# Optimization experiments

Measured on AMD Instinct MI355X. Metric: run time of the kernel, lower is better.

Reference implementation:

```python
import jax, jax.numpy as jnp
import numpy as np

N = 100000      # nodes
E = 1600000     # edges
F_IN = 64       # node_features
F_OUT = 32      # output_size


def _cheb2(H, row, col, w_norm, theta, bias):
    # ChebConv K=2, sym normalization, lambda_max=2 (GCLSTM default):
    # L_hat = L - I = -D^{-1/2} A D^{-1/2}, so T0 = H, T1 = -A_norm H
    agg = jax.ops.segment_sum(w_norm[:, None] * H[col], row, num_segments=N)  # [N, F_OUT]
    return H @ theta[0] - agg @ theta[1] + bias


def setup_inputs() -> dict:
    key = jax.random.key(0)
    ks = jax.random.split(key, 24)
    inp = {}
    inp["x"] = jax.random.normal(ks[0], (N, F_IN), jnp.float32)
    inp["edge_index"] = jax.random.randint(ks[1], (2, E), 0, N)
    inp["edge_weight"] = jax.random.uniform(ks[2], (E,), jnp.float32)
    inp["h"] = jax.random.normal(ks[3], (N, F_OUT), jnp.float32)
    inp["c"] = jax.random.normal(ks[4], (N, F_OUT), jnp.float32)
    s_in = float(1.0 / np.sqrt(F_IN))
    s_out = float(1.0 / np.sqrt(F_OUT))
    i = 5
    for g in "ifco":
        inp[f"W_{g}"] = jax.random.uniform(ks[i], (F_IN, F_OUT), jnp.float32, -s_in, s_in); i += 1
        inp[f"b_{g}"] = jax.random.uniform(ks[i], (1, F_OUT), jnp.float32, -s_in, s_in); i += 1
        inp[f"theta_{g}"] = jax.random.uniform(ks[i], (2, F_OUT, F_OUT), jnp.float32, -s_out, s_out); i += 1
        inp[f"cb_{g}"] = jax.random.uniform(ks[i], (F_OUT,), jnp.float32, -s_out, s_out); i += 1
    inp["W_lin"] = jax.random.uniform(ks[i], (F_OUT, 1), jnp.float32, -s_out, s_out); i += 1
    inp["b_lin"] = jax.random.uniform(ks[i], (1,), jnp.float32, -s_out, s_out)
    return inp


def reference(x, edge_index, edge_weight, h, c,
              W_i, b_i, theta_i, cb_i,
              W_f, b_f, theta_f, cb_f,
              W_c, b_c, theta_c, cb_c,
              W_o, b_o, theta_o, cb_o,
              W_lin, b_lin):
    row, col = edge_index[0], edge_index[1]
    # symmetric normalization of edge weights (get_laplacian 'sym')
    deg = jax.ops.segment_sum(edge_weight, row, num_segments=N)
    dis = jnp.where(deg > 0, jax.lax.rsqrt(jnp.where(deg > 0, deg, 1.0)), 0.0)
    w_norm = dis[row] * edge_weight * dis[col]  # [E]
    # GCLSTM gates: input x through dense W, hidden h through ChebConv
    I = jax.nn.sigmoid(x @ W_i + _cheb2(h, row, col, w_norm, theta_i, cb_i) + b_i)
    Fg = jax.nn.sigmoid(x @ W_f + _cheb2(h, row, col, w_norm, theta_f, cb_f) + b_f)
    T = jnp.tanh(x @ W_c + _cheb2(h, row, col, w_norm, theta_c, cb_c) + b_c)
    C = Fg * c + I * T
    O = jax.nn.sigmoid(x @ W_o + _cheb2(h, row, col, w_norm, theta_o, cb_o) + b_o)
    H = O * jnp.tanh(C)
    # wrapper head: relu then Linear(out, 1)
    return jax.nn.relu(H) @ W_lin + b_lin  # [N, 1]
```

## Files before the change

### kernel.cpp

```cpp
#include <hip/hip_runtime.h>
#include <math.h>

#define NN 100000
#define NE 1600000
#define BSH 7
#define BMSK 127
#define NBUK 782
#define EPB 2048
#define NEB 782
#define CAPH 1536

typedef __attribute__((ext_vector_type(8))) short bf16x8;
typedef __attribute__((ext_vector_type(4))) float f32x4;

#define MFMA(A, B, C) __builtin_amdgcn_mfma_f32_16x16x32_bf16(A, B, C, 0, 0, 0)

__device__ __forceinline__ float sigm(float z) { return 1.0f / (1.0f + expf(-z)); }

__device__ __forceinline__ void split1(float v, unsigned short* hi, unsigned short* lo) {
  unsigned u = __float_as_uint(v);
  *hi = (unsigned short)(u >> 16);
  float hf = __uint_as_float(u & 0xFFFF0000u);
  float lf = v - hf;
  *lo = (unsigned short)(__float_as_uint(lf) >> 16);
}

__device__ __forceinline__ void split8(const float* f, bf16x8* hi, bf16x8* lo) {
#pragma unroll
  for (int j = 0; j < 8; ++j) {
    unsigned short h, l;
    split1(f[j], &h, &l);
    (*hi)[j] = (short)h;
    (*lo)[j] = (short)l;
  }
}

__device__ __forceinline__ bf16x8 as_bf16x8(uint4 q) {
  union { uint4 q; bf16x8 v; } u;
  u.q = q;
  return u.v;
}

__device__ __forceinline__ void load8(const float4* p, int idx4, float* f) {
  float4 a = p[idx4];
  float4 b = p[idx4 + 1];
  f[0] = a.x; f[1] = a.y; f[2] = a.z; f[3] = a.w;
  f[4] = b.x; f[5] = b.y; f[6] = b.z; f[7] = b.w;
}


__global__ __launch_bounds__(256) void k_p1(const int* __restrict__ row,
                                            unsigned short* __restrict__ counts) {
  __shared__ int hist[NBUK];
  for (int i = threadIdx.x; i < NBUK; i += 256) hist[i] = 0;
  __syncthreads();
  int e0 = blockIdx.x * EPB;
  int e1 = min(e0 + EPB, NE);
  for (int e = e0 + (int)threadIdx.x; e < e1; e += 256)
    atomicAdd(&hist[row[e] >> BSH], 1);
  __syncthreads();
  for (int i = threadIdx.x; i < NBUK; i += 256)
    counts[blockIdx.x * NBUK + i] = (unsigned short)hist[i];
}

__global__ __launch_bounds__(1024) void k_s1(unsigned short* __restrict__ counts,
                                             int* __restrict__ total) {
  __shared__ int s[1024];
  int b = blockIdx.x;
  int t = threadIdx.x;
  int v = (t < NEB) ? (int)counts[t * NBUK + b] : 0;
  s[t] = v;
  __syncthreads();
  for (int o = 1; o < 1024; o <<= 1) {
    int a = (t >= o) ? s[t - o] : 0;
    __syncthreads();
    s[t] += a;
    __syncthreads();
  }
  if (t < NEB) counts[t * NBUK + b] = (unsigned short)(s[t] - v);
  if (t == 1023) total[b] = s[1023];
}

struct S2PParams {
  const int* total;
  int* bases;
  const float* W[4];
  const float* T0[4];
  const float* T1[4];
  const float* b[4];
  const float* cb[4];
  uint4* fh;
  uint4* fl;
  float* bias;
};

__global__ __launch_bounds__(1024) void k_s2p(S2PParams pp) {
  int t = threadIdx.x;
  if (blockIdx.x == 0) {
    __shared__ int s[1024];
    int v = (t < NBUK) ? pp.total[t] : 0;
    s[t] = v;
    __syncthreads();
    for (int o = 1; o < 1024; o <<= 1) {
      int a = (t >= o) ? s[t - o] : 0;
      __syncthreads();
      s[t] += a;
      __syncthreads();
    }
    if (t < NBUK) pp.bases[t] = s[t] - v;
    if (t == 0) pp.bases[NBUK] = NE;
    if (t >= 896) {
      int i = t - 896;
      pp.bias[i] = pp.b[i >> 5][i & 31] + pp.cb[i >> 5][i & 31];
    }
    return;
  }
  int idx = (blockIdx.x - 1) * 1024 + t;
  if (idx < 2048) {
    int T = idx >> 6;
    int lane = idx & 63;
    int ncol = ((T & 7) * 16) + (lane & 15);
    int g = ncol >> 5;
    int c = ncol & 31;
    int kq = (lane >> 4) * 8;
    const float* mat;
    int kbase;
    if (T < 16) { mat = pp.W[g]; kbase = (T >> 3) * 32 + kq; }
    else if (T < 24) { mat = pp.T0[g]; kbase = kq; }
    else { mat = pp.T1[g]; kbase = kq; }
    unsigned hw[4], lw[4];
#pragma unroll
    for (int jj = 0; jj < 4; ++jj) {
      unsigned short h0, l0, h1, l1;
      split1(mat[(kbase + 2 * jj) * 32 + c], &h0, &l0);
      split1(mat[(kbase + 2 * jj + 1) * 32 + c], &h1, &l1);
      hw[jj] = (unsigned)h0 | ((unsigned)h1 << 16);
      lw[jj] = (unsigned)l0 | ((unsigned)l1 << 16);
    }
    pp.fh[idx] = make_uint4(hw[0], hw[1], hw[2], hw[3]);
    pp.fl[idx] = make_uint4(lw[0], lw[1], lw[2], lw[3]);
  }
}

__global__ __launch_bounds__(256) void k_p2(const int* __restrict__ row,
                                            const int* __restrict__ col,
                                            const float* __restrict__ ew,
                                            const unsigned short* __restrict__ rel,
                                            const int* __restrict__ bases,
                                            int2* __restrict__ colw) {
  __shared__ int cursor[NBUK];
  for (int i = threadIdx.x; i < NBUK; i += 256)
    cursor[i] = bases[i] + (int)rel[blockIdx.x * NBUK + i];
  __syncthreads();
  int e0 = blockIdx.x * EPB;
  int e1 = min(e0 + EPB, NE);
  for (int e = e0 + (int)threadIdx.x; e < e1; e += 256) {
    int r = row[e];
    int c = col[e];
    float w = ew[e];
    int slot = atomicAdd(&cursor[r >> BSH], 1);
    colw[slot] = make_int2(c | ((r & BMSK) << 17), __float_as_int(w));
  }
}

__global__ __launch_bounds__(256) void k_deg(const int* __restrict__ bases,
                                             const int2* __restrict__ colw,
                                             float* __restrict__ dis) {
  __shared__ float dg[64];
  int j = blockIdx.x;
  int b = j >> 1;
  int hf = j & 1;
  int nbase = (b << BSH) + (hf << 6);
  if (nbase >= NN) return;
  int t = threadIdx.x;
  if (t < 64) dg[t] = 0.0f;
  __syncthreads();
  int base = bases[b];
  int M = bases[b + 1] - base;
  for (int i = t; i < M; i += 256) {
    int2 e = colw[base + i];
    int rl = e.x >> 17;
    if ((rl >> 6) == hf) atomicAdd(&dg[rl & 63], __int_as_float(e.y));
  }
  __syncthreads();
  int node = nbase + t;
  if (t < 64 && node < NN) {
    float d = dg[t];
    dis[node] = d > 0.0f ? rsqrtf(d) : 0.0f;
  }
}

struct FusedParams {
  const float4* x4;
  const float4* h4;
  const float* cst;
  const int* bases;
  const int2* colw;
  const float* dis;
  const uint4* fh;
  const uint4* fl;
  const float* bias;
  const float* wlin;
  const float* blin;
  float* out;
};

__device__ __forceinline__ void accrowL(const FusedParams& p, int quad, int2 cw,
                                        float* acc) {
  const float4* hp = p.h4 + (cw.x * 8 + quad * 2);
  float4 a0 = hp[0], a1 = hp[1];
  float w = __int_as_float(cw.y);
  acc[0] = fmaf(w, a0.x, acc[0]); acc[1] = fmaf(w, a0.y, acc[1]);
  acc[2] = fmaf(w, a0.z, acc[2]); acc[3] = fmaf(w, a0.w, acc[3]);
  acc[4] = fmaf(w, a1.x, acc[4]); acc[5] = fmaf(w, a1.y, acc[5]);
  acc[6] = fmaf(w, a1.z, acc[6]); acc[7] = fmaf(w, a1.w, acc[7]);
}

__global__ __launch_bounds__(256) void k_fused(FusedParams p) {
  __shared__ int2 stage[CAPH];
  __shared__ int cnt[64], excl[64], cursor[64];
  __shared__ int s[256];
  const int t = threadIdx.x;
  const int jb = blockIdx.x;
  const int b = jb >> 1;
  const int hf = jb & 1;
  const int nbase = (b << BSH) + (hf << 6);
  if (nbase >= NN) return;
  if (t < 64) cnt[t] = 0;
  __syncthreads();

  const int base = p.bases[b];
  const int M = p.bases[b + 1] - base;
  for (int i = t; i < M; i += 256) {
    int cx = p.colw[base + i].x;
    int rl = cx >> 17;
    if ((rl >> 6) == hf) atomicAdd(&cnt[rl & 63], 1);
  }
  __syncthreads();
  {
    int v = (t < 64) ? cnt[t] : 0;
    s[t] = v;
    __syncthreads();
    for (int o = 1; o < 64; o <<= 1) {
      int a = (t >= o) ? s[t - o] : 0;
      __syncthreads();
      s[t] += a;
      __syncthreads();
    }
    if (t < 64) {
      excl[t] = s[t] - v;
      cursor[t] = s[t] - v;
    }
  }
  __syncthreads();
  for (int i = t; i < M; i += 256) {
    int2 e = p.colw[base + i];
    int rl = e.x >> 17;
    if ((rl >> 6) == hf) {
      int c = e.x & 0x1FFFF;
      float w = __int_as_float(e.y) * p.dis[c];
      int slot = atomicAdd(&cursor[rl & 63], 1);
      if (slot < CAPH) stage[slot] = make_int2(c, __float_as_int(w));
    }
  }
  __syncthreads();

  const int lane = t & 63;
  const int wv = t >> 6;
  const int mr = lane & 15;
  const int quad = lane >> 4;
  const int m0 = nbase + wv * 16;
  int m = m0 + mr;
  if (m >= NN) m = NN - 1;
  const int rlh = m - nbase;

  bf16x8 xh[2], xl[2], hh, hl, gh, gl;
  float f[8];
#pragma unroll
  for (int kt = 0; kt < 2; ++kt) {
    load8(p.x4, (m * 64 + kt * 32 + quad * 8) >> 2, f);
    split8(f, &xh[kt], &xl[kt]);
  }
  load8(p.h4, (m * 32 + quad * 8) >> 2, f);
  split8(f, &hh, &hl);

  float fa[8] = {0.f, 0.f, 0.f, 0.f, 0.f, 0.f, 0.f, 0.f};
  float fb[8] = {0.f, 0.f, 0.f, 0.f, 0.f, 0.f, 0.f, 0.f};
  {
    int s0 = excl[rlh];
    int rem = cnt[rlh];
    int j = 0;
    for (; j + 3 < rem; j += 4) {
      int2 w0 = stage[s0 + j], w1 = stage[s0 + j + 1];
      int2 w2 = stage[s0 + j + 2], w3 = stage[s0 + j + 3];
      const float4* h0 = p.h4 + (w0.x * 8 + quad * 2);
      const float4* h1 = p.h4 + (w1.x * 8 + quad * 2);
      const float4* h2 = p.h4 + (w2.x * 8 + quad * 2);
      const float4* h3 = p.h4 + (w3.x * 8 + quad * 2);
      float4 a0 = h0[0], a1 = h0[1];
      float4 b0 = h1[0], b1 = h1[1];
      float4 c0 = h2[0], c1 = h2[1];
      float4 d0 = h3[0], d1 = h3[1];
      float f0 = __int_as_float(w0.y), f1 = __int_as_float(w1.y);
      float f2 = __int_as_float(w2.y), f3 = __int_as_float(w3.y);
      fa[0] = fmaf(f0, a0.x, fa[0]); fa[1] = fmaf(f0, a0.y, fa[1]);
      fa[2] = fmaf(f0, a0.z, fa[2]); fa[3] = fmaf(f0, a0.w, fa[3]);
      fa[4] = fmaf(f0, a1.x, fa[4]); fa[5] = fmaf(f0, a1.y, fa[5]);
      fa[6] = fmaf(f0, a1.z, fa[6]); fa[7] = fmaf(f0, a1.w, fa[7]);
      fb[0] = fmaf(f1, b0.x, fb[0]); fb[1] = fmaf(f1, b0.y, fb[1]);
      fb[2] = fmaf(f1, b0.z, fb[2]); fb[3] = fmaf(f1, b0.w, fb[3]);
      fb[4] = fmaf(f1, b1.x, fb[4]); fb[5] = fmaf(f1, b1.y, fb[5]);
      fb[6] = fmaf(f1, b1.z, fb[6]); fb[7] = fmaf(f1, b1.w, fb[7]);
      fa[0] = fmaf(f2, c0.x, fa[0]); fa[1] = fmaf(f2, c0.y, fa[1]);
      fa[2] = fmaf(f2, c0.z, fa[2]); fa[3] = fmaf(f2, c0.w, fa[3]);
      fa[4] = fmaf(f2, c1.x, fa[4]); fa[5] = fmaf(f2, c1.y, fa[5]);
      fa[6] = fmaf(f2, c1.z, fa[6]); fa[7] = fmaf(f2, c1.w, fa[7]);
      fb[0] = fmaf(f3, d0.x, fb[0]); fb[1] = fmaf(f3, d0.y, fb[1]);
      fb[2] = fmaf(f3, d0.z, fb[2]); fb[3] = fmaf(f3, d0.w, fb[3]);
      fb[4] = fmaf(f3, d1.x, fb[4]); fb[5] = fmaf(f3, d1.y, fb[5]);
      fb[6] = fmaf(f3, d1.z, fb[6]); fb[7] = fmaf(f3, d1.w, fb[7]);
    }
    for (; j < rem; ++j) accrowL(p, quad, stage[s0 + j], fa);
  }
  {
    float dn = -p.dis[m];
#pragma unroll
    for (int j = 0; j < 8; ++j) f[j] = dn * (fa[j] + fb[j]);
    split8(f, &gh, &gl);
  }

  float wl0 = p.wlin[mr];
  float wl1 = p.wlin[mr + 16];
  float bl = p.blin[0];

  f32x4 acc[8];
#pragma unroll 2
  for (int nt = 0; nt < 8; ++nt) {
    float bv = p.bias[nt * 16 + mr];
    f32x4 a;
    a[0] = bv; a[1] = bv; a[2] = bv; a[3] = bv;
    bf16x8 b0h = as_bf16x8(p.fh[nt * 64 + lane]);
    bf16x8 b0l = as_bf16x8(p.fl[nt * 64 + lane]);
    bf16x8 b1h = as_bf16x8(p.fh[(8 + nt) * 64 + lane]);
    bf16x8 b1l = as_bf16x8(p.fl[(8 + nt) * 64 + lane]);
    bf16x8 t0h = as_bf16x8(p.fh[(16 + nt) * 64 + lane]);
    bf16x8 t0l = as_bf16x8(p.fl[(16 + nt) * 64 + lane]);
    bf16x8 t1h = as_bf16x8(p.fh[(24 + nt) * 64 + lane]);
    bf16x8 t1l = as_bf16x8(p.fl[(24 + nt) * 64 + lane]);
    a = MFMA(xh[0], b0h, a); a = MFMA(xh[0], b0l, a); a = MFMA(xl[0], b0h, a);
    a = MFMA(xh[1], b1h, a); a = MFMA(xh[1], b1l, a); a = MFMA(xl[1], b1h, a);
    a = MFMA(hh, t0h, a);    a = MFMA(hh, t0l, a);    a = MFMA(hl, t0h, a);
    a = MFMA(gh, t1h, a);    a = MFMA(gh, t1l, a);    a = MFMA(gl, t1h, a);
    acc[nt] = a;
  }

#pragma unroll
  for (int r = 0; r < 4; ++r) {
    int node = m0 + quad * 4 + r;
    int nc = node < NN ? node : NN - 1;
    float c0 = p.cst[nc * 32 + mr];
    float c1 = p.cst[nc * 32 + 16 + mr];
    float I0 = sigm(acc[0][r]), I1 = sigm(acc[1][r]);
    float F0 = sigm(acc[2][r]), F1 = sigm(acc[3][r]);
    float T0 = tanhf(acc[4][r]), T1 = tanhf(acc[5][r]);
    float O0 = sigm(acc[6][r]), O1 = sigm(acc[7][r]);
    float C0 = fmaf(F0, c0, I0 * T0);
    float C1 = fmaf(F1, c1, I1 * T1);
    float H0 = O0 * tanhf(C0);
    float H1 = O1 * tanhf(C1);
    float part = fmaf(fmaxf(H0, 0.f), wl0, fmaxf(H1, 0.f) * wl1);
#pragma unroll
    for (int sh = 1; sh < 16; sh <<= 1) part += __shfl_xor(part, sh, 64);
    if (mr == 0 && node < NN) p.out[node] = part + bl;
  }
}

extern "C" void kernel_launch(void* const* d_in, const int* in_sizes, int n_in,
                              void* d_out, int out_size, void* d_ws, size_t ws_size,
                              hipStream_t stream) {
  const float* x = (const float*)d_in[0];
  const int* row = (const int*)d_in[1];
  const int* col = row + NE;
  const float* ew = (const float*)d_in[2];
  const float* h = (const float*)d_in[3];
  const float* c = (const float*)d_in[4];

  float* ws = (float*)d_ws;
  float* dis = ws;
  int* total = (int*)(ws + 100000);
  int* bases = (int*)(ws + 100782);
  unsigned short* counts = (unsigned short*)(ws + 101568);
  uint4* fh = (uint4*)(ws + 407332);
  uint4* fl = (uint4*)(ws + 415524);
  float* biasws = ws + 423716;
  int2* colw = (int2*)(ws + 423844);

  k_p1<<<NEB, 256, 0, stream>>>(row, counts);
  k_s1<<<NBUK, 1024, 0, stream>>>(counts, total);

  S2PParams sp;
  sp.total = total;
  sp.bases = bases;
  for (int g = 0; g < 4; ++g) {
    sp.W[g] = (const float*)d_in[5 + 4 * g];
    sp.b[g] = (const float*)d_in[6 + 4 * g];
    sp.T0[g] = (const float*)d_in[7 + 4 * g];
    sp.T1[g] = sp.T0[g] + 1024;
    sp.cb[g] = (const float*)d_in[8 + 4 * g];
  }
  sp.fh = fh;
  sp.fl = fl;
  sp.bias = biasws;
  k_s2p<<<3, 1024, 0, stream>>>(sp);

  k_p2<<<NEB, 256, 0, stream>>>(row, col, ew, counts, bases, colw);
  k_deg<<<2 * NBUK, 256, 0, stream>>>(bases, colw, dis);

  FusedParams fp;
  fp.x4 = (const float4*)x;
  fp.h4 = (const float4*)h;
  fp.cst = c;
  fp.bases = bases;
  fp.colw = colw;
  fp.dis = dis;
  fp.fh = fh;
  fp.fl = fl;
  fp.bias = biasws;
  fp.wlin = (const float*)d_in[21];
  fp.blin = (const float*)d_in[22];
  fp.out = (float*)d_out;
  k_fused<<<2 * NBUK, 256, 0, stream>>>(fp);
}
```

Measured before the change: 265.2 us.

## Replace prefix-sum bucket sort with fixed-capacity buckets and global atomic cursors

```diff
diff --git a/kernel.cpp b/kernel.cpp
--- a/kernel.cpp
+++ b/kernel.cpp
@@ -3,12 +3,12 @@
 
 #define NN 100000
 #define NE 1600000
-#define BSH 7
-#define BMSK 127
-#define NBUK 782
-#define EPB 2048
-#define NEB 782
-#define CAPH 1536
+#define BSH 6
+#define BMSK 63
+#define NBUK 1563
+#define CAP 1280
+#define NSB 391
+#define EPC 4096
 
 typedef __attribute__((ext_vector_type(8))) short bf16x8;
 typedef __attribute__((ext_vector_type(4))) float f32x4;
@@ -49,144 +49,102 @@
 }
 
 
-__global__ __launch_bounds__(256) void k_p1(const int* __restrict__ row,
-                                            unsigned short* __restrict__ counts) {
+__global__ __launch_bounds__(256) void k_scat(const int* __restrict__ row,
+                                              const int* __restrict__ col,
+                                              const float* __restrict__ ew,
+                                              int* __restrict__ cursor,
+                                              int2* __restrict__ colw) {
   __shared__ int hist[NBUK];
-  for (int i = threadIdx.x; i < NBUK; i += 256) hist[i] = 0;
-  __syncthreads();
-  int e0 = blockIdx.x * EPB;
-  int e1 = min(e0 + EPB, NE);
-  for (int e = e0 + (int)threadIdx.x; e < e1; e += 256)
+  const int t = threadIdx.x;
+  const int bid = blockIdx.x;
+  for (int i = t; i < NBUK; i += 256) hist[i] = 0;
+  __syncthreads();
+  const int e0 = bid * EPC;
+  const int e1 = min(e0 + EPC, NE);
+  for (int e = e0 + t; e < e1; e += 256)
     atomicAdd(&hist[row[e] >> BSH], 1);
   __syncthreads();
-  for (int i = threadIdx.x; i < NBUK; i += 256)
-    counts[blockIdx.x * NBUK + i] = (unsigned short)hist[i];
-}
-
-__global__ __launch_bounds__(1024) void k_s1(unsigned short* __restrict__ counts,
-                                             int* __restrict__ total) {
-  __shared__ int s[1024];
-  int b = blockIdx.x;
-  int t = threadIdx.x;
-  int v = (t < NEB) ? (int)counts[t * NBUK + b] : 0;
-  s[t] = v;
-  __syncthreads();
-  for (int o = 1; o < 1024; o <<= 1) {
-    int a = (t >= o) ? s[t - o] : 0;
-    __syncthreads();
-    s[t] += a;
-    __syncthreads();
-  }
-  if (t < NEB) counts[t * NBUK + b] = (unsigned short)(s[t] - v);
-  if (t == 1023) total[b] = s[1023];
-}
-
-struct S2PParams {
-  const int* total;
-  int* bases;
+  const int off = (bid * 61) % NBUK;
+  for (int i0 = t; i0 < NBUK; i0 += 256) {
+    int i = i0 + off;
+    if (i >= NBUK) i -= NBUK;
+    int h = hist[i];
+    if (h > 0) hist[i] = atomicAdd(&cursor[i], h);
+  }
+  __syncthreads();
+  for (int e = e0 + t; e < e1; e += 256) {
+    int r = row[e];
+    int c = col[e];
+    float w = ew[e];
+    int b = r >> BSH;
+    int slot = atomicAdd(&hist[b], 1);
+    if (slot < CAP)
+      colw[b * CAP + slot] = make_int2(c | ((r & BMSK) << 17), __float_as_int(w));
+  }
+}
+
+struct DegParams {
+  const int* cursor;
+  const int2* colw;
+  float* dis;
   const float* W[4];
   const float* T0[4];
   const float* T1[4];
-  const float* b[4];
+  const float* bsrc[4];
   const float* cb[4];
   uint4* fh;
   uint4* fl;
   float* bias;
 };
 
-__global__ __launch_bounds__(1024) void k_s2p(S2PParams pp) {
-  int t = threadIdx.x;
-  if (blockIdx.x == 0) {
-    __shared__ int s[1024];
-    int v = (t < NBUK) ? pp.total[t] : 0;
-    s[t] = v;
-    __syncthreads();
-    for (int o = 1; o < 1024; o <<= 1) {
-      int a = (t >= o) ? s[t - o] : 0;
-      __syncthreads();
-      s[t] += a;
-      __syncthreads();
-    }
-    if (t < NBUK) pp.bases[t] = s[t] - v;
-    if (t == 0) pp.bases[NBUK] = NE;
-    if (t >= 896) {
-      int i = t - 896;
-      pp.bias[i] = pp.b[i >> 5][i & 31] + pp.cb[i >> 5][i & 31];
+__global__ __launch_bounds__(256) void k_deg(DegParams p) {
+  const int t = threadIdx.x;
+  const int bid = blockIdx.x;
+  if (bid >= NBUK) {
+    int ex = bid - NBUK;
+    if (ex < 8) {
+      int idx = ex * 256 + t;
+      int T = idx >> 6;
+      int lane = idx & 63;
+      int ncol = ((T & 7) * 16) + (lane & 15);
+      int g = ncol >> 5;
+      int c = ncol & 31;
+      int kq = (lane >> 4) * 8;
+      const float* mat;
+      int kbase;
+      if (T < 16) { mat = p.W[g]; kbase = (T >> 3) * 32 + kq; }
+      else if (T < 24) { mat = p.T0[g]; kbase = kq; }
+      else { mat = p.T1[g]; kbase = kq; }
+      unsigned hw[4], lw[4];
+#pragma unroll
+      for (int jj = 0; jj < 4; ++jj) {
+        unsigned short h0, l0, h1, l1;
+        split1(mat[(kbase + 2 * jj) * 32 + c], &h0, &l0);
+        split1(mat[(kbase + 2 * jj + 1) * 32 + c], &h1, &l1);
+        hw[jj] = (unsigned)h0 | ((unsigned)h1 << 16);
+        lw[jj] = (unsigned)l0 | ((unsigned)l1 << 16);
+      }
+      p.fh[idx] = make_uint4(hw[0], hw[1], hw[2], hw[3]);
+      p.fl[idx] = make_uint4(lw[0], lw[1], lw[2], lw[3]);
+    } else if (t < 128) {
+      p.bias[t] = p.bsrc[t >> 5][t & 31] + p.cb[t >> 5][t & 31];
     }
     return;
   }
-  int idx = (blockIdx.x - 1) * 1024 + t;
-  if (idx < 2048) {
-    int T = idx >> 6;
-    int lane = idx & 63;
-    int ncol = ((T & 7) * 16) + (lane & 15);
-    int g = ncol >> 5;
-    int c = ncol & 31;
-    int kq = (lane >> 4) * 8;
-    const float* mat;
-    int kbase;
-    if (T < 16) { mat = pp.W[g]; kbase = (T >> 3) * 32 + kq; }
-    else if (T < 24) { mat = pp.T0[g]; kbase = kq; }
-    else { mat = pp.T1[g]; kbase = kq; }
-    unsigned hw[4], lw[4];
-#pragma unroll
-    for (int jj = 0; jj < 4; ++jj) {
-      unsigned short h0, l0, h1, l1;
-      split1(mat[(kbase + 2 * jj) * 32 + c], &h0, &l0);
-      split1(mat[(kbase + 2 * jj + 1) * 32 + c], &h1, &l1);
-      hw[jj] = (unsigned)h0 | ((unsigned)h1 << 16);
-      lw[jj] = (unsigned)l0 | ((unsigned)l1 << 16);
-    }
-    pp.fh[idx] = make_uint4(hw[0], hw[1], hw[2], hw[3]);
-    pp.fl[idx] = make_uint4(lw[0], lw[1], lw[2], lw[3]);
-  }
-}
-
-__global__ __launch_bounds__(256) void k_p2(const int* __restrict__ row,
-                                            const int* __restrict__ col,
-                                            const float* __restrict__ ew,
-                                            const unsigned short* __restrict__ rel,
-                                            const int* __restrict__ bases,
-                                            int2* __restrict__ colw) {
-  __shared__ int cursor[NBUK];
-  for (int i = threadIdx.x; i < NBUK; i += 256)
-    cursor[i] = bases[i] + (int)rel[blockIdx.x * NBUK + i];
-  __syncthreads();
-  int e0 = blockIdx.x * EPB;
-  int e1 = min(e0 + EPB, NE);
-  for (int e = e0 + (int)threadIdx.x; e < e1; e += 256) {
-    int r = row[e];
-    int c = col[e];
-    float w = ew[e];
-    int slot = atomicAdd(&cursor[r >> BSH], 1);
-    colw[slot] = make_int2(c | ((r & BMSK) << 17), __float_as_int(w));
-  }
-}
-
-__global__ __launch_bounds__(256) void k_deg(const int* __restrict__ bases,
-                                             const int2* __restrict__ colw,
-                                             float* __restrict__ dis) {
   __shared__ float dg[64];
-  int j = blockIdx.x;
-  int b = j >> 1;
-  int hf = j & 1;
-  int nbase = (b << BSH) + (hf << 6);
-  if (nbase >= NN) return;
-  int t = threadIdx.x;
   if (t < 64) dg[t] = 0.0f;
   __syncthreads();
-  int base = bases[b];
-  int M = bases[b + 1] - base;
+  const int M = min(p.cursor[bid], CAP);
+  const int base = bid * CAP;
   for (int i = t; i < M; i += 256) {
-    int2 e = colw[base + i];
-    int rl = e.x >> 17;
-    if ((rl >> 6) == hf) atomicAdd(&dg[rl & 63], __int_as_float(e.y));
-  }
-  __syncthreads();
-  int node = nbase + t;
+    int2 e = p.colw[base + i];
+    atomicAdd(&dg[e.x >> 17], __int_as_float(e.y));
+  }
+  __syncthreads();
+  int node = (bid << BSH) + t;
   if (t < 64 && node < NN) {
     float d = dg[t];
-    dis[node] = d > 0.0f ? rsqrtf(d) : 0.0f;
+    p.dis[node] = d > 0.0f ? rsqrtf(d) : 0.0f;
   }
 }
 
@@ -194,7 +152,7 @@
   const float4* x4;
   const float4* h4;
   const float* cst;
-  const int* bases;
+  const int* cursor;
   const int2* colw;
   const float* dis;
   const uint4* fh;
@@ -205,37 +163,20 @@
   float* out;
 };
 
-__device__ __forceinline__ void accrowL(const FusedParams& p, int quad, int2 cw,
-                                        float* acc) {
-  const float4* hp = p.h4 + (cw.x * 8 + quad * 2);
-  float4 a0 = hp[0], a1 = hp[1];
-  float w = __int_as_float(cw.y);
-  acc[0] = fmaf(w, a0.x, acc[0]); acc[1] = fmaf(w, a0.y, acc[1]);
-  acc[2] = fmaf(w, a0.z, acc[2]); acc[3] = fmaf(w, a0.w, acc[3]);
-  acc[4] = fmaf(w, a1.x, acc[4]); acc[5] = fmaf(w, a1.y, acc[5]);
-  acc[6] = fmaf(w, a1.z, acc[6]); acc[7] = fmaf(w, a1.w, acc[7]);
-}
-
 __global__ __launch_bounds__(256) void k_fused(FusedParams p) {
-  __shared__ int2 stage[CAPH];
-  __shared__ int cnt[64], excl[64], cursor[64];
+  __shared__ int2 stage[CAP];
+  __shared__ int cnt[64], excl[64], cur64[64];
   __shared__ int s[256];
   const int t = threadIdx.x;
-  const int jb = blockIdx.x;
-  const int b = jb >> 1;
-  const int hf = jb & 1;
-  const int nbase = (b << BSH) + (hf << 6);
-  if (nbase >= NN) return;
+  const int b = blockIdx.x;
+  const int nbase = b << BSH;
   if (t < 64) cnt[t] = 0;
   __syncthreads();
 
-  const int base = p.bases[b];
-  const int M = p.bases[b + 1] - base;
-  for (int i = t; i < M; i += 256) {
-    int cx = p.colw[base + i].x;
-    int rl = cx >> 17;
-    if ((rl >> 6) == hf) atomicAdd(&cnt[rl & 63], 1);
-  }
+  const int base = b * CAP;
+  const int M = min(p.cursor[b], CAP);
+  for (int i = t; i < M; i += 256)
+    atomicAdd(&cnt[p.colw[base + i].x >> 17], 1);
   __syncthreads();
   {
     int v = (t < 64) ? cnt[t] : 0;
@@ -249,19 +190,17 @@
     }
     if (t < 64) {
       excl[t] = s[t] - v;
-      cursor[t] = s[t] - v;
+      cur64[t] = s[t] - v;
     }
   }
   __syncthreads();
   for (int i = t; i < M; i += 256) {
     int2 e = p.colw[base + i];
     int rl = e.x >> 17;
-    if ((rl >> 6) == hf) {
-      int c = e.x & 0x1FFFF;
-      float w = __int_as_float(e.y) * p.dis[c];
-      int slot = atomicAdd(&cursor[rl & 63], 1);
-      if (slot < CAPH) stage[slot] = make_int2(c, __float_as_int(w));
-    }
+    int c = e.x & 0x1FFFF;
+    float w = __int_as_float(e.y) * p.dis[c];
+    int slot = atomicAdd(&cur64[rl], 1);
+    stage[slot] = make_int2(c, __float_as_int(w));
   }
   __syncthreads();
 
@@ -320,7 +259,16 @@
       fb[4] = fmaf(f3, d1.x, fb[4]); fb[5] = fmaf(f3, d1.y, fb[5]);
       fb[6] = fmaf(f3, d1.z, fb[6]); fb[7] = fmaf(f3, d1.w, fb[7]);
     }
-    for (; j < rem; ++j) accrowL(p, quad, stage[s0 + j], fa);
+    for (; j < rem; ++j) {
+      int2 cw = stage[s0 + j];
+      const float4* hp = p.h4 + (cw.x * 8 + quad * 2);
+      float4 a0 = hp[0], a1 = hp[1];
+      float w = __int_as_float(cw.y);
+      fa[0] = fmaf(w, a0.x, fa[0]); fa[1] = fmaf(w, a0.y, fa[1]);
+      fa[2] = fmaf(w, a0.z, fa[2]); fa[3] = fmaf(w, a0.w, fa[3]);
+      fa[4] = fmaf(w, a1.x, fa[4]); fa[5] = fmaf(w, a1.y, fa[5]);
+      fa[6] = fmaf(w, a1.z, fa[6]); fa[7] = fmaf(w, a1.w, fa[7]);
+    }
   }
   {
     float dn = -p.dis[m];
@@ -387,40 +335,36 @@
 
   float* ws = (float*)d_ws;
   float* dis = ws;
-  int* total = (int*)(ws + 100000);
-  int* bases = (int*)(ws + 100782);
-  unsigned short* counts = (unsigned short*)(ws + 101568);
-  uint4* fh = (uint4*)(ws + 407332);
-  uint4* fl = (uint4*)(ws + 415524);
-  float* biasws = ws + 423716;
-  int2* colw = (int2*)(ws + 423844);
-
-  k_p1<<<NEB, 256, 0, stream>>>(row, counts);
-  k_s1<<<NBUK, 1024, 0, stream>>>(counts, total);
-
-  S2PParams sp;
-  sp.total = total;
-  sp.bases = bases;
+  int* cursor = (int*)(ws + 100000);
+  uint4* fh = (uint4*)(ws + 101568);
+  uint4* fl = (uint4*)(ws + 109760);
+  float* biasws = ws + 117952;
+  int2* colw = (int2*)(ws + 118080);
+
+  hipMemsetAsync(cursor, 0, NBUK * sizeof(int), stream);
+  k_scat<<<NSB, 256, 0, stream>>>(row, col, ew, cursor, colw);
+
+  DegParams dp;
+  dp.cursor = cursor;
+  dp.colw = colw;
+  dp.dis = dis;
   for (int g = 0; g < 4; ++g) {
-    sp.W[g] = (const float*)d_in[5 + 4 * g];
-    sp.b[g] = (const float*)d_in[6 + 4 * g];
-    sp.T0[g] = (const float*)d_in[7 + 4 * g];
-    sp.T1[g] = sp.T0[g] + 1024;
-    sp.cb[g] = (const float*)d_in[8 + 4 * g];
-  }
-  sp.fh = fh;
-  sp.fl = fl;
-  sp.bias = biasws;
-  k_s2p<<<3, 1024, 0, stream>>>(sp);
-
-  k_p2<<<NEB, 256, 0, stream>>>(row, col, ew, counts, bases, colw);
-  k_deg<<<2 * NBUK, 256, 0, stream>>>(bases, colw, dis);
+    dp.W[g] = (const float*)d_in[5 + 4 * g];
+    dp.bsrc[g] = (const float*)d_in[6 + 4 * g];
+    dp.T0[g] = (const float*)d_in[7 + 4 * g];
+    dp.T1[g] = dp.T0[g] + 1024;
+    dp.cb[g] = (const float*)d_in[8 + 4 * g];
+  }
+  dp.fh = fh;
+  dp.fl = fl;
+  dp.bias = biasws;
+  k_deg<<<NBUK + 9, 256, 0, stream>>>(dp);
 
   FusedParams fp;
   fp.x4 = (const float4*)x;
   fp.h4 = (const float4*)h;
   fp.cst = c;
-  fp.bases = bases;
+  fp.cursor = cursor;
   fp.colw = colw;
   fp.dis = dis;
   fp.fh = fh;
@@ -429,5 +373,5 @@
   fp.wlin = (const float*)d_in[21];
   fp.blin = (const float*)d_in[22];
   fp.out = (float*)d_out;
-  k_fused<<<2 * NBUK, 256, 0, stream>>>(fp);
-}
+  k_fused<<<NBUK, 256, 0, stream>>>(fp);
+}
```

Measured after the change: 260.8 us. About the same (-1.6%).
